# Optimization experiments

Measured on AMD Instinct MI355X. Metric: run time of the kernel, lower is better.

The kernel has to match this reference:

```python
import jax, jax.numpy as jnp
import numpy as np

E_NUM, R_NUM, D, B = 100000, 200, 128, 4096


def setup_inputs() -> dict:
    key = jax.random.key(0)
    k = jax.random.split(key, 7)
    return {
        "h": jax.random.randint(k[0], (B,), 0, E_NUM),
        "r": jax.random.randint(k[1], (B,), 0, R_NUM),
        "pos_t": jax.random.randint(k[2], (B,), 0, E_NUM),
        "neg_t": jax.random.randint(k[3], (B,), 0, E_NUM),
        # xavier-normal-ish init scales
        "entity_embed": jax.random.normal(k[4], (E_NUM, D), jnp.float32) * 0.12,
        "relation_embed": jax.random.normal(k[5], (R_NUM, D), jnp.float32) * 0.12,
        "trans_M": jax.random.normal(k[6], (R_NUM, D * D), jnp.float32) * 0.011,
    }


def reference(h, r, pos_t, neg_t, entity_embed, relation_embed, trans_M):
    h_e = entity_embed[h]            # [B, D]
    pos_e = entity_embed[pos_t]      # [B, D]
    neg_e = entity_embed[neg_t]      # [B, D]
    r_e = relation_embed[r]          # [B, D]
    W_r = trans_M[r].reshape(-1, D, D)  # [B, D, D]
    # row-vector @ matrix per sample: (1xD) @ (DxD) -> D
    trans_h = jnp.einsum("bd,bde->be", h_e, W_r)
    trans_pos = jnp.einsum("bd,bde->be", pos_e, W_r)
    trans_neg = jnp.einsum("bd,bde->be", neg_e, W_r)
    return (trans_h, r_e, trans_pos, trans_neg)
```

## Files before the change

kernel.cpp:

```cpp
#include <hip/hip_runtime.h>

#define DDIM   128
#define QCOL   32
#define SCH    21
#define MROWS  64
#define XSTRIDE 136
#define SEGCAP 96

typedef __attribute__((ext_vector_type(8))) short bf16x8;
typedef __attribute__((ext_vector_type(4))) float f32x4;

static __device__ inline unsigned short f2b(float f) {
    unsigned u = __float_as_uint(f);
    u += 0x7fff + ((u >> 16) & 1);
    return (unsigned short)(u >> 16);
}

__global__ __launch_bounds__(256) void transr_mfma(
    const int* __restrict__ h, const int* __restrict__ r,
    const int* __restrict__ pos_t, const int* __restrict__ neg_t,
    const float* __restrict__ ent, const float* __restrict__ rel,
    const float* __restrict__ M, float* __restrict__ out,
    int B, int R)
{
    const int bid  = blockIdx.x;
    const int rb   = bid % R;
    const int qc   = bid / R;
    const int t  = threadIdx.x;
    const int wv = t >> 6;
    const int ln = t & 63;

    __shared__ __align__(16) unsigned short Xl[MROWS * XSTRIDE];
    __shared__ __align__(16) unsigned short Wt[QCOL  * XSTRIDE];
    __shared__ int seg[4][SEGCAP];
    __shared__ int wcnt[4];
    __shared__ int list_s[4 * SEGCAP];

    {
        const float* __restrict__ Wg = M + (size_t)rb * DDIM * DDIM + qc * QCOL;
        const int g   = t >> 4;
        const int nl0 = t & 15;
        #pragma unroll
        for (int i = 0; i < 2; ++i) {
            const int nloc = nl0 + i * 16;
            bf16x8 v;
            #pragma unroll
            for (int jj = 0; jj < 8; ++jj)
                v[jj] = (short)f2b(Wg[(size_t)(g * 8 + jj) * DDIM + nloc]);
            *(bf16x8*)(&Wt[nloc * XSTRIDE + g * 8]) = v;
        }
    }

    int segn = 0;
    const int qlen  = B >> 2;
    const int qbase = wv * qlen;
    for (int i0 = 0; i0 < qlen; i0 += 64) {
        const int  idx = qbase + i0 + ln;
        const bool f   = (idx < B) && (r[idx] == rb);
        const unsigned long long m = __ballot(f);
        if (f) {
            const int p = segn + __popcll(m & ((1ull << ln) - 1ull));
            if (p < SEGCAP) seg[wv][p] = idx;
        }
        segn += __popcll(m);
    }
    if (ln == 0) wcnt[wv] = min(segn, SEGCAP);
    __syncthreads();

    const int c0 = wcnt[0], c1 = wcnt[1], c2 = wcnt[2], c3 = wcnt[3];
    const int cum1 = c0, cum2 = c0 + c1, cum3 = c0 + c1 + c2;
    const int cnt  = cum3 + c3;
    if (cnt == 0) return;

    for (int lin = t; lin < cnt; lin += 256) {
        int w, k;
        if      (lin < cum1) { w = 0; k = lin;        }
        else if (lin < cum2) { w = 1; k = lin - cum1; }
        else if (lin < cum3) { w = 2; k = lin - cum2; }
        else                 { w = 3; k = lin - cum3; }
        list_s[lin] = seg[w][k];
    }
    __syncthreads();

    for (int lin = t; lin < cnt * (QCOL / 4); lin += 256) {
        const int j  = lin >> 3;
        const int c4 = lin & 7;
        const float4 v = *(const float4*)(rel + (size_t)rb * DDIM + qc * QCOL + c4 * 4);
        *(float4*)(out + (size_t)B * DDIM + (size_t)list_s[j] * DDIM + qc * QCOL + c4 * 4) = v;
    }

    for (int ch = 0; ch < cnt; ch += SCH) {
        const int ccnt = min(SCH, cnt - ch);
        const int rows_valid = 3 * ccnt;

        for (int lin = t; lin < MROWS * 16; lin += 256) {
            const int row = lin >> 4;
            const int g   = lin & 15;
            int j = row / 3;
            const int v = row - 3 * j;
            if (j >= ccnt) j = ccnt - 1;
            const int sidx = list_s[ch + j];
            const int eid  = (v == 0) ? h[sidx] : (v == 1) ? pos_t[sidx] : neg_t[sidx];
            const float4 a = *(const float4*)(ent + (size_t)eid * DDIM + g * 8);
            const float4 b = *(const float4*)(ent + (size_t)eid * DDIM + g * 8 + 4);
            bf16x8 x;
            x[0] = (short)f2b(a.x); x[1] = (short)f2b(a.y);
            x[2] = (short)f2b(a.z); x[3] = (short)f2b(a.w);
            x[4] = (short)f2b(b.x); x[5] = (short)f2b(b.y);
            x[6] = (short)f2b(b.z); x[7] = (short)f2b(b.w);
            *(bf16x8*)(&Xl[row * XSTRIDE + g * 8]) = x;
        }
        __syncthreads();

        const int mt = wv;
        f32x4 acc0 = {0.f, 0.f, 0.f, 0.f};
        f32x4 acc1 = {0.f, 0.f, 0.f, 0.f};
        const int lr = ln & 15;
        const int lg = ln >> 4;
        #pragma unroll
        for (int ks = 0; ks < 4; ++ks) {
            const int g = ks * 4 + lg;
            const bf16x8 a  = *(const bf16x8*)(&Xl[(mt * 16 + lr) * XSTRIDE + g * 8]);
            const bf16x8 b0 = *(const bf16x8*)(&Wt[(0 * 16 + lr) * XSTRIDE + g * 8]);
            const bf16x8 b1 = *(const bf16x8*)(&Wt[(1 * 16 + lr) * XSTRIDE + g * 8]);
            acc0 = __builtin_amdgcn_mfma_f32_16x16x32_bf16(a, b0, acc0, 0, 0, 0);
            acc1 = __builtin_amdgcn_mfma_f32_16x16x32_bf16(a, b1, acc1, 0, 0, 0);
        }

        const size_t BD = (size_t)B * DDIM;
        #pragma unroll
        for (int q = 0; q < 4; ++q) {
            const int row = mt * 16 + lg * 4 + q;
            if (row < rows_valid) {
                const int jj = row / 3;
                const int v  = row - 3 * jj;
                const size_t s = (size_t)list_s[ch + jj];
                float* bp = (v == 0) ? out : (v == 1) ? (out + 2 * BD) : (out + 3 * BD);
                bp += s * DDIM + qc * QCOL + lr;
                bp[0]  = acc0[q];
                bp[16] = acc1[q];
            }
        }
        __syncthreads();
    }
}

extern "C" void kernel_launch(void* const* d_in, const int* in_sizes, int n_in,
                              void* d_out, int out_size, void* d_ws, size_t ws_size,
                              hipStream_t stream) {
    const int*   h     = (const int*)d_in[0];
    const int*   r     = (const int*)d_in[1];
    const int*   pos_t = (const int*)d_in[2];
    const int*   neg_t = (const int*)d_in[3];
    const float* ent   = (const float*)d_in[4];
    const float* rel   = (const float*)d_in[5];
    const float* M     = (const float*)d_in[6];
    float*       out   = (float*)d_out;

    const int B = in_sizes[0];
    const int R = in_sizes[5] / DDIM;

    transr_mfma<<<dim3(R * 4), dim3(256), 0, stream>>>(
        h, r, pos_t, neg_t, ent, rel, M, out, B, R);
}
```

Before: 17.23 us.

## Pre-bucket samples by relation with atomic kernel instead of per-block scans

Result: slower. 23.28 us (+35.2%).

```diff
diff --git a/kernel.cpp b/kernel.cpp
--- a/kernel.cpp
+++ b/kernel.cpp
@@ -1,11 +1,11 @@
 #include <hip/hip_runtime.h>
 
-#define DDIM   128
-#define QCOL   32
-#define SCH    21
-#define MROWS  64
+#define DDIM    128
+#define QCOL    32
+#define SCH     21
+#define MROWS   64
 #define XSTRIDE 136
-#define SEGCAP 96
+#define BSTRIDE 128
 
 typedef __attribute__((ext_vector_type(8))) short bf16x8;
 typedef __attribute__((ext_vector_type(4))) float f32x4;
@@ -16,25 +16,37 @@
     return (unsigned short)(u >> 16);
 }
 
+__global__ __launch_bounds__(256) void bucket_kernel(
+    const int* __restrict__ r, int B, int* __restrict__ cnt, int* __restrict__ bucket)
+{
+    const int i = blockIdx.x * 256 + threadIdx.x;
+    if (i < B) {
+        const int rel  = r[i];
+        const int slot = atomicAdd(&cnt[rel], 1);
+        if (slot < BSTRIDE) bucket[rel * BSTRIDE + slot] = i;
+    }
+}
+
 __global__ __launch_bounds__(256) void transr_mfma(
-    const int* __restrict__ h, const int* __restrict__ r,
-    const int* __restrict__ pos_t, const int* __restrict__ neg_t,
+    const int* __restrict__ h, const int* __restrict__ pos_t, const int* __restrict__ neg_t,
     const float* __restrict__ ent, const float* __restrict__ rel,
     const float* __restrict__ M, float* __restrict__ out,
+    const int* __restrict__ cntg, const int* __restrict__ bucket,
     int B, int R)
 {
-    const int bid  = blockIdx.x;
-    const int rb   = bid % R;
-    const int qc   = bid / R;
-    const int t  = threadIdx.x;
-    const int wv = t >> 6;
-    const int ln = t & 63;
+    const int bid = blockIdx.x;
+    const int rb  = bid % R;
+    const int qc  = bid / R;
+    const int t   = threadIdx.x;
 
     __shared__ __align__(16) unsigned short Xl[MROWS * XSTRIDE];
     __shared__ __align__(16) unsigned short Wt[QCOL  * XSTRIDE];
-    __shared__ int seg[4][SEGCAP];
-    __shared__ int wcnt[4];
-    __shared__ int list_s[4 * SEGCAP];
+    __shared__ int list_s[BSTRIDE];
+    __shared__ int eid_s[3 * BSTRIDE];
+
+    const int cnt = min(cntg[rb], BSTRIDE);
+
+    if (t < BSTRIDE) list_s[t] = bucket[rb * BSTRIDE + t];
 
     {
         const float* __restrict__ Wg = M + (size_t)rb * DDIM * DDIM + qc * QCOL;
@@ -50,37 +62,14 @@
             *(bf16x8*)(&Wt[nloc * XSTRIDE + g * 8]) = v;
         }
     }
-
-    int segn = 0;
-    const int qlen  = B >> 2;
-    const int qbase = wv * qlen;
-    for (int i0 = 0; i0 < qlen; i0 += 64) {
-        const int  idx = qbase + i0 + ln;
-        const bool f   = (idx < B) && (r[idx] == rb);
-        const unsigned long long m = __ballot(f);
-        if (f) {
-            const int p = segn + __popcll(m & ((1ull << ln) - 1ull));
-            if (p < SEGCAP) seg[wv][p] = idx;
-        }
-        segn += __popcll(m);
-    }
-    if (ln == 0) wcnt[wv] = min(segn, SEGCAP);
     __syncthreads();
 
-    const int c0 = wcnt[0], c1 = wcnt[1], c2 = wcnt[2], c3 = wcnt[3];
-    const int cum1 = c0, cum2 = c0 + c1, cum3 = c0 + c1 + c2;
-    const int cnt  = cum3 + c3;
-    if (cnt == 0) return;
-
-    for (int lin = t; lin < cnt; lin += 256) {
-        int w, k;
-        if      (lin < cum1) { w = 0; k = lin;        }
-        else if (lin < cum2) { w = 1; k = lin - cum1; }
-        else if (lin < cum3) { w = 2; k = lin - cum2; }
-        else                 { w = 3; k = lin - cum3; }
-        list_s[lin] = seg[w][k];
+    for (int i = t; i < 3 * cnt; i += 256) {
+        const int j = i / 3;
+        const int v = i - 3 * j;
+        const int sidx = list_s[j];
+        eid_s[i] = (v == 0) ? h[sidx] : (v == 1) ? pos_t[sidx] : neg_t[sidx];
     }
-    __syncthreads();
 
     for (int lin = t; lin < cnt * (QCOL / 4); lin += 256) {
         const int j  = lin >> 3;
@@ -88,6 +77,7 @@
         const float4 v = *(const float4*)(rel + (size_t)rb * DDIM + qc * QCOL + c4 * 4);
         *(float4*)(out + (size_t)B * DDIM + (size_t)list_s[j] * DDIM + qc * QCOL + c4 * 4) = v;
     }
+    __syncthreads();
 
     for (int ch = 0; ch < cnt; ch += SCH) {
         const int ccnt = min(SCH, cnt - ch);
@@ -96,11 +86,8 @@
         for (int lin = t; lin < MROWS * 16; lin += 256) {
             const int row = lin >> 4;
             const int g   = lin & 15;
-            int j = row / 3;
-            const int v = row - 3 * j;
-            if (j >= ccnt) j = ccnt - 1;
-            const int sidx = list_s[ch + j];
-            const int eid  = (v == 0) ? h[sidx] : (v == 1) ? pos_t[sidx] : neg_t[sidx];
+            const int rowg = min(3 * ch + row, 3 * cnt - 1);
+            const int eid  = eid_s[rowg];
             const float4 a = *(const float4*)(ent + (size_t)eid * DDIM + g * 8);
             const float4 b = *(const float4*)(ent + (size_t)eid * DDIM + g * 8 + 4);
             bf16x8 x;
@@ -112,15 +99,16 @@
         }
         __syncthreads();
 
-        const int mt = wv;
+        const int wv = t >> 6;
+        const int ln = t & 63;
+        const int lr = ln & 15;
+        const int lg = ln >> 4;
         f32x4 acc0 = {0.f, 0.f, 0.f, 0.f};
         f32x4 acc1 = {0.f, 0.f, 0.f, 0.f};
-        const int lr = ln & 15;
-        const int lg = ln >> 4;
         #pragma unroll
         for (int ks = 0; ks < 4; ++ks) {
             const int g = ks * 4 + lg;
-            const bf16x8 a  = *(const bf16x8*)(&Xl[(mt * 16 + lr) * XSTRIDE + g * 8]);
+            const bf16x8 a  = *(const bf16x8*)(&Xl[(wv * 16 + lr) * XSTRIDE + g * 8]);
             const bf16x8 b0 = *(const bf16x8*)(&Wt[(0 * 16 + lr) * XSTRIDE + g * 8]);
             const bf16x8 b1 = *(const bf16x8*)(&Wt[(1 * 16 + lr) * XSTRIDE + g * 8]);
             acc0 = __builtin_amdgcn_mfma_f32_16x16x32_bf16(a, b0, acc0, 0, 0, 0);
@@ -130,7 +118,7 @@
         const size_t BD = (size_t)B * DDIM;
         #pragma unroll
         for (int q = 0; q < 4; ++q) {
-            const int row = mt * 16 + lg * 4 + q;
+            const int row = wv * 16 + lg * 4 + q;
             if (row < rows_valid) {
                 const int jj = row / 3;
                 const int v  = row - 3 * jj;
@@ -160,6 +148,11 @@
     const int B = in_sizes[0];
     const int R = in_sizes[5] / DDIM;
 
+    int* cnt    = (int*)d_ws;
+    int* bucket = cnt + 256;
+
+    hipMemsetAsync(cnt, 0, 256 * sizeof(int), stream);
+    bucket_kernel<<<dim3((B + 255) / 256), dim3(256), 0, stream>>>(r, B, cnt, bucket);
     transr_mfma<<<dim3(R * 4), dim3(256), 0, stream>>>(
-        h, r, pos_t, neg_t, ent, rel, M, out, B, R);
+        h, pos_t, neg_t, ent, rel, M, out, cnt, bucket, B, R);
 }
```

## Split output columns into 8 slices, vectorize relation scan, overlap weight load

Applied to the files above, without the earlier changes.

Result: slower. 20.31 us (+17.9%).

```diff
diff --git a/kernel.cpp b/kernel.cpp
--- a/kernel.cpp
+++ b/kernel.cpp
@@ -1,11 +1,13 @@
 #include <hip/hip_runtime.h>
 
-#define DDIM   128
-#define QCOL   32
-#define SCH    21
-#define MROWS  64
+#define DDIM    128
+#define NS      8
+#define SCOL    16
+#define SCH     21
+#define MROWS   64
 #define XSTRIDE 136
-#define SEGCAP 96
+#define WSTRIDE 136
+#define SEGCAP  96
 
 typedef __attribute__((ext_vector_type(8))) short bf16x8;
 typedef __attribute__((ext_vector_type(4))) float f32x4;
@@ -23,48 +25,54 @@
     const float* __restrict__ M, float* __restrict__ out,
     int B, int R)
 {
-    const int bid  = blockIdx.x;
-    const int rb   = bid % R;
-    const int qc   = bid / R;
-    const int t  = threadIdx.x;
-    const int wv = t >> 6;
-    const int ln = t & 63;
+    const int bid = blockIdx.x;
+    const int rb  = bid % R;
+    const int qc  = bid / R;
+    const int t   = threadIdx.x;
+    const int wvid = t >> 6;
+    const int ln   = t & 63;
 
     __shared__ __align__(16) unsigned short Xl[MROWS * XSTRIDE];
-    __shared__ __align__(16) unsigned short Wt[QCOL  * XSTRIDE];
+    __shared__ __align__(16) unsigned short Wt[SCOL  * WSTRIDE];
     __shared__ int seg[4][SEGCAP];
     __shared__ int wcnt[4];
     __shared__ int list_s[4 * SEGCAP];
 
-    {
-        const float* __restrict__ Wg = M + (size_t)rb * DDIM * DDIM + qc * QCOL;
-        const int g   = t >> 4;
-        const int nl0 = t & 15;
+    const int g  = t >> 4;
+    const int nl = t & 15;
+    const float* __restrict__ Wg = M + (size_t)rb * DDIM * DDIM + qc * SCOL + nl;
+    float wreg[8];
+    #pragma unroll
+    for (int j = 0; j < 8; ++j) wreg[j] = Wg[(size_t)(g * 8 + j) * DDIM];
+
+    int segn = 0;
+    const int qlen4  = B >> 4;
+    const int qbase4 = wvid * qlen4;
+    const int4* __restrict__ r4 = (const int4*)r;
+    for (int i0 = 0; i0 < qlen4; i0 += 64) {
+        const int  e4 = qbase4 + i0 + ln;
+        const int4 rv = r4[e4];
+        const int  ib = e4 << 2;
         #pragma unroll
-        for (int i = 0; i < 2; ++i) {
-            const int nloc = nl0 + i * 16;
-            bf16x8 v;
-            #pragma unroll
-            for (int jj = 0; jj < 8; ++jj)
-                v[jj] = (short)f2b(Wg[(size_t)(g * 8 + jj) * DDIM + nloc]);
-            *(bf16x8*)(&Wt[nloc * XSTRIDE + g * 8]) = v;
+        for (int j = 0; j < 4; ++j) {
+            const int  rj = (j == 0) ? rv.x : (j == 1) ? rv.y : (j == 2) ? rv.z : rv.w;
+            const bool f  = (rj == rb);
+            const unsigned long long m = __ballot(f);
+            if (f) {
+                const int p = segn + __popcll(m & ((1ull << ln) - 1ull));
+                if (p < SEGCAP) seg[wvid][p] = ib + j;
+            }
+            segn += __popcll(m);
         }
     }
+    if (ln == 0) wcnt[wvid] = min(segn, SEGCAP);
 
-    int segn = 0;
-    const int qlen  = B >> 2;
-    const int qbase = wv * qlen;
-    for (int i0 = 0; i0 < qlen; i0 += 64) {
-        const int  idx = qbase + i0 + ln;
-        const bool f   = (idx < B) && (r[idx] == rb);
-        const unsigned long long m = __ballot(f);
-        if (f) {
-            const int p = segn + __popcll(m & ((1ull << ln) - 1ull));
-            if (p < SEGCAP) seg[wv][p] = idx;
-        }
-        segn += __popcll(m);
+    {
+        bf16x8 wv8;
+        #pragma unroll
+        for (int j = 0; j < 8; ++j) wv8[j] = (short)f2b(wreg[j]);
+        *(bf16x8*)(&Wt[nl * WSTRIDE + g * 8]) = wv8;
     }
-    if (ln == 0) wcnt[wv] = min(segn, SEGCAP);
     __syncthreads();
 
     const int c0 = wcnt[0], c1 = wcnt[1], c2 = wcnt[2], c3 = wcnt[3];
@@ -82,66 +90,60 @@
     }
     __syncthreads();
 
-    for (int lin = t; lin < cnt * (QCOL / 4); lin += 256) {
-        const int j  = lin >> 3;
-        const int c4 = lin & 7;
-        const float4 v = *(const float4*)(rel + (size_t)rb * DDIM + qc * QCOL + c4 * 4);
-        *(float4*)(out + (size_t)B * DDIM + (size_t)list_s[j] * DDIM + qc * QCOL + c4 * 4) = v;
-    }
-
+    const int lr = ln & 15;
+    const int lg = ln >> 4;
     for (int ch = 0; ch < cnt; ch += SCH) {
-        const int ccnt = min(SCH, cnt - ch);
-        const int rows_valid = 3 * ccnt;
+        const int rows_valid = 3 * (min(SCH, cnt - ch));
 
         for (int lin = t; lin < MROWS * 16; lin += 256) {
-            const int row = lin >> 4;
-            const int g   = lin & 15;
-            int j = row / 3;
-            const int v = row - 3 * j;
-            if (j >= ccnt) j = ccnt - 1;
-            const int sidx = list_s[ch + j];
+            const int row  = lin >> 4;
+            const int kg   = lin & 15;
+            const int rowg = min(3 * ch + row, 3 * cnt - 1);
+            const int jj   = rowg / 3;
+            const int v    = rowg - 3 * jj;
+            const int sidx = list_s[jj];
             const int eid  = (v == 0) ? h[sidx] : (v == 1) ? pos_t[sidx] : neg_t[sidx];
-            const float4 a = *(const float4*)(ent + (size_t)eid * DDIM + g * 8);
-            const float4 b = *(const float4*)(ent + (size_t)eid * DDIM + g * 8 + 4);
+            const float4 a = *(const float4*)(ent + (size_t)eid * DDIM + kg * 8);
+            const float4 b = *(const float4*)(ent + (size_t)eid * DDIM + kg * 8 + 4);
             bf16x8 x;
             x[0] = (short)f2b(a.x); x[1] = (short)f2b(a.y);
             x[2] = (short)f2b(a.z); x[3] = (short)f2b(a.w);
             x[4] = (short)f2b(b.x); x[5] = (short)f2b(b.y);
             x[6] = (short)f2b(b.z); x[7] = (short)f2b(b.w);
-            *(bf16x8*)(&Xl[row * XSTRIDE + g * 8]) = x;
+            *(bf16x8*)(&Xl[row * XSTRIDE + kg * 8]) = x;
         }
         __syncthreads();
 
-        const int mt = wv;
         f32x4 acc0 = {0.f, 0.f, 0.f, 0.f};
-        f32x4 acc1 = {0.f, 0.f, 0.f, 0.f};
-        const int lr = ln & 15;
-        const int lg = ln >> 4;
         #pragma unroll
         for (int ks = 0; ks < 4; ++ks) {
-            const int g = ks * 4 + lg;
-            const bf16x8 a  = *(const bf16x8*)(&Xl[(mt * 16 + lr) * XSTRIDE + g * 8]);
-            const bf16x8 b0 = *(const bf16x8*)(&Wt[(0 * 16 + lr) * XSTRIDE + g * 8]);
-            const bf16x8 b1 = *(const bf16x8*)(&Wt[(1 * 16 + lr) * XSTRIDE + g * 8]);
+            const int kg = ks * 4 + lg;
+            const bf16x8 a  = *(const bf16x8*)(&Xl[(wvid * 16 + lr) * XSTRIDE + kg * 8]);
+            const bf16x8 b0 = *(const bf16x8*)(&Wt[lr * WSTRIDE + kg * 8]);
             acc0 = __builtin_amdgcn_mfma_f32_16x16x32_bf16(a, b0, acc0, 0, 0, 0);
-            acc1 = __builtin_amdgcn_mfma_f32_16x16x32_bf16(a, b1, acc1, 0, 0, 0);
         }
 
         const size_t BD = (size_t)B * DDIM;
         #pragma unroll
         for (int q = 0; q < 4; ++q) {
-            const int row = mt * 16 + lg * 4 + q;
+            const int row = wvid * 16 + lg * 4 + q;
             if (row < rows_valid) {
-                const int jj = row / 3;
-                const int v  = row - 3 * jj;
-                const size_t s = (size_t)list_s[ch + jj];
+                const int rowg = 3 * ch + row;
+                const int jj   = rowg / 3;
+                const int v    = rowg - 3 * jj;
+                const size_t s = (size_t)list_s[jj];
                 float* bp = (v == 0) ? out : (v == 1) ? (out + 2 * BD) : (out + 3 * BD);
-                bp += s * DDIM + qc * QCOL + lr;
-                bp[0]  = acc0[q];
-                bp[16] = acc1[q];
+                bp[s * DDIM + qc * SCOL + lr] = acc0[q];
             }
         }
         __syncthreads();
+    }
+
+    for (int lin = t; lin < cnt * (SCOL / 4); lin += 256) {
+        const int j  = lin >> 2;
+        const int c4 = lin & 3;
+        const float4 v = *(const float4*)(rel + (size_t)rb * DDIM + qc * SCOL + c4 * 4);
+        *(float4*)(out + (size_t)B * DDIM + (size_t)list_s[j] * DDIM + qc * SCOL + c4 * 4) = v;
     }
 }
 
@@ -160,6 +162,6 @@
     const int B = in_sizes[0];
     const int R = in_sizes[5] / DDIM;
 
-    transr_mfma<<<dim3(R * 4), dim3(256), 0, stream>>>(
+    transr_mfma<<<dim3(R * NS), dim3(256), 0, stream>>>(
         h, r, pos_t, neg_t, ent, rel, M, out, B, R);
 }
```
